# Performance work log

Hardware: AMD Instinct MI355X
Metric: run time of the kernel (lower is better)

## Reference

```python
import jax, jax.numpy as jnp
import numpy as np

B, T, D = 4, 2048, 1024
DEPTH = 4
LEAF_DIM = 256
NUM_LEAVES = 2 ** DEPTH          # 16
NUM_NODES = NUM_LEAVES - 1       # 15


def _uniform(key, shape, scale):
    s = 1.0 / np.sqrt(scale)
    return jax.random.uniform(key, shape, minval=-s, maxval=s, dtype=jnp.float32)


def setup_inputs() -> dict:
    key = jax.random.key(0)
    ks = jax.random.split(key, 8)
    x = jax.random.normal(ks[0], (B, T, D), dtype=jnp.float32)
    # gate params: Dense(1) per internal node, level-order layout
    node_w = _uniform(ks[1], (NUM_NODES, D), D)
    node_b = _uniform(ks[2], (NUM_NODES,), D)
    # leaf MLP params: D -> LEAF_DIM -> D, stacked over leaves
    w1 = _uniform(ks[3], (NUM_LEAVES, D, LEAF_DIM), D)
    b1 = _uniform(ks[4], (NUM_LEAVES, LEAF_DIM), D)
    w2 = _uniform(ks[5], (NUM_LEAVES, LEAF_DIM, D), LEAF_DIM)
    b2 = _uniform(ks[6], (NUM_LEAVES, D), LEAF_DIM)
    return {"x": x, "node_w": node_w, "node_b": node_b,
            "w1": w1, "b1": b1, "w2": w2, "b2": b2, "training": 0}


def _leaf_probs(x, node_w, node_b, depth):
    # gate activations for all internal nodes at once: [B,T,NUM_NODES]
    c = jax.nn.sigmoid(jnp.einsum('btd,nd->btn', x, node_w) + node_b)
    probs = jnp.ones(c.shape[:-1] + (1,), dtype=c.dtype)
    for m in range(depth):
        start = 2 ** m - 1
        cl = c[..., start:start + 2 ** m]          # gates at level m: [B,T,2^m]
        # left child gets c, right child gets (1-c); interleave preserves
        # the recursion's n -> (2n, 2n+1) indexing
        probs = jnp.stack([probs * cl, probs * (1.0 - cl)], axis=-1)
        probs = probs.reshape(probs.shape[:-2] + (-1,))
    return probs                                   # [B,T,NUM_LEAVES]


def reference(x, node_w, node_b, w1, b1, w2, b2, training):
    num_leaves = w1.shape[0]
    depth = int(np.log2(num_leaves))
    probs = _leaf_probs(x, node_w, node_b, depth)          # [B,T,L]
    # all leaf MLP hidden layers as one batched GEMM
    h = jax.nn.relu(jnp.einsum('btd,ldh->btlh', x, w1) + b1)
    # weight hidden by leaf probability, then contract l and h together so the
    # [B,T,L,D] per-leaf output is never materialized
    h = h * probs[..., None]
    out = jnp.einsum('btlh,lhd->btd', h, w2)
    out = out + jnp.einsum('btl,ld->btd', probs, b2)
    return out
```

## Files before the change

### kernel.cpp

```cpp
#include <hip/hip_runtime.h>
#include <stdint.h>

typedef unsigned short ushort_t;
typedef __bf16 bf16x8 __attribute__((ext_vector_type(8)));
typedef float f32x4 __attribute__((ext_vector_type(4)));

#define M_TOK 8192
#define K1 1024
#define N1 4096
#define K2 4160
#define N2 1024

template <int V> struct ic { static constexpr int value = V; };

__device__ __forceinline__ ushort_t f2bf(float f) {
  union { float f; unsigned u; } v; v.f = f;
  unsigned u = v.u;
  u += 0x7FFFu + ((u >> 16) & 1u);
  return (ushort_t)(u >> 16);
}

__device__ __forceinline__ void gload16(const void* g, void* l) {
  __builtin_amdgcn_global_load_lds((__attribute__((address_space(1))) void*)g,
                                   (__attribute__((address_space(3))) void*)l,
                                   16, 0, 0);
}

__global__ __launch_bounds__(256) void k_prep(
    const float* __restrict__ x, const float* __restrict__ node_w,
    const float* __restrict__ node_b, const float* __restrict__ w1,
    const float* __restrict__ w2, const float* __restrict__ b2,
    ushort_t* __restrict__ xb, float* __restrict__ probs,
    ushort_t* __restrict__ w1t, ushort_t* __restrict__ w2t,
    ushort_t* __restrict__ hp) {
  __shared__ ushort_t tile[64][68];
  const int b = blockIdx.x;
  if (b < 1024) {
    const int tr = threadIdx.x >> 4, tc = (threadIdx.x & 15) * 4;
    const int l = b >> 6, rem = b & 63;
    const int kt = rem >> 2, ht = rem & 3;
    const float* in = w1 + (size_t)l * K1 * 256;
#pragma unroll
    for (int rr = 0; rr < 4; ++rr) {
      int r = tr + rr * 16;
      float4 v = *(const float4*)(in + (size_t)(kt * 64 + r) * 256 + ht * 64 + tc);
      tile[r][tc+0] = f2bf(v.x); tile[r][tc+1] = f2bf(v.y);
      tile[r][tc+2] = f2bf(v.z); tile[r][tc+3] = f2bf(v.w);
    }
    __syncthreads();
#pragma unroll
    for (int rr = 0; rr < 4; ++rr) {
      int oh = tr + rr * 16;
      ushort4 o;
      o.x = tile[tc+0][oh]; o.y = tile[tc+1][oh];
      o.z = tile[tc+2][oh]; o.w = tile[tc+3][oh];
      *(ushort4*)(w1t + (size_t)(l * 256 + ht * 64 + oh) * K1 + kt * 64 + tc) = o;
    }
  } else if (b < 2048) {
    const int tr = threadIdx.x >> 4, tc = (threadIdx.x & 15) * 4;
    const int bb = b - 1024;
    const int l = bb >> 6, rem = bb & 63;
    const int ht = rem >> 4, dt = rem & 15;
    const float* in = w2 + (size_t)l * 256 * N2;
#pragma unroll
    for (int rr = 0; rr < 4; ++rr) {
      int r = tr + rr * 16;
      float4 v = *(const float4*)(in + (size_t)(ht * 64 + r) * N2 + dt * 64 + tc);
      tile[r][tc+0] = f2bf(v.x); tile[r][tc+1] = f2bf(v.y);
      tile[r][tc+2] = f2bf(v.z); tile[r][tc+3] = f2bf(v.w);
    }
    __syncthreads();
#pragma unroll
    for (int rr = 0; rr < 4; ++rr) {
      int od = tr + rr * 16;
      ushort4 o;
      o.x = tile[tc+0][od]; o.y = tile[tc+1][od];
      o.z = tile[tc+2][od]; o.w = tile[tc+3][od];
      *(ushort4*)(w2t + (size_t)(dt * 64 + od) * K2 + l * 256 + ht * 64 + tc) = o;
    }
  } else if (b < 2304) {
    int tid = (b - 2048) * 256 + threadIdx.x;
    int d = tid >> 6, cc = tid & 63;
    float v = (cc < 16) ? b2[cc * N2 + d] : 0.f;
    w2t[(size_t)d * K2 + 4096 + cc] = f2bf(v);
  } else {
    const int wid = threadIdx.x >> 6, lane = threadIdx.x & 63;
    const int t = (b - 2304) * 4 + wid;
    const float* xr = x + (size_t)t * K1;
    float xv[16];
#pragma unroll
    for (int j = 0; j < 4; ++j) {
      float4 v = *(const float4*)(xr + j * 256 + lane * 4);
      xv[4*j+0] = v.x; xv[4*j+1] = v.y; xv[4*j+2] = v.z; xv[4*j+3] = v.w;
    }
    ushort_t* xbr = xb + (size_t)t * K1;
#pragma unroll
    for (int j = 0; j < 4; ++j) {
      ushort4 o;
      o.x = f2bf(xv[4*j+0]); o.y = f2bf(xv[4*j+1]);
      o.z = f2bf(xv[4*j+2]); o.w = f2bf(xv[4*j+3]);
      *(ushort4*)(xbr + j * 256 + lane * 4) = o;
    }
    float c[15];
#pragma unroll
    for (int n = 0; n < 15; ++n) {
      float s = 0.f;
      const float* wr = node_w + n * K1;
#pragma unroll
      for (int j = 0; j < 4; ++j) {
        float4 w = *(const float4*)(wr + j * 256 + lane * 4);
        s += xv[4*j+0]*w.x + xv[4*j+1]*w.y + xv[4*j+2]*w.z + xv[4*j+3]*w.w;
      }
#pragma unroll
      for (int off = 32; off > 0; off >>= 1) s += __shfl_xor(s, off);
      float z = s + node_b[n];
      c[n] = 1.f / (1.f + __expf(-z));
    }
    if (lane < 16) {
      float p = 1.f;
#pragma unroll
      for (int m = 0; m < 4; ++m) {
        int jm = lane >> (4 - m);
        int node = (1 << m) - 1 + jm;
        int bit = (lane >> (3 - m)) & 1;
        p *= bit ? (1.f - c[node]) : c[node];
      }
      probs[t * 16 + lane] = p;
      hp[(size_t)t * K2 + 4096 + lane] = f2bf(p);
    }
    if (lane < 48) hp[(size_t)t * K2 + 4112 + lane] = 0;
  }
}

template <int NT, int LDA, int LDB, int BM, int BN, int THREADS, int MODE>
__global__ __launch_bounds__(THREADS, 4) void k_gemm(
    const ushort_t* __restrict__ A, const ushort_t* __restrict__ Bt,
    const float* __restrict__ probs, const float* __restrict__ b1,
    ushort_t* __restrict__ hp, float* __restrict__ out, int ntn) {
  constexpr int NWAVE = THREADS / 64;
  constexpr int WN = (BN == 256) ? 4 : 2;
  constexpr int WM = NWAVE / WN;
  constexpr int HA = BM / 2;
  constexpr int FH = HA / (WM * 16);
  constexpr int BHR = BN / 2;
  constexpr int ATILE = BM * 64;
  constexpr int BBYTES = BHR * 64;
  constexpr int BOFF = 2 * ATILE;
  constexpr int AR = (BM * 64) / (THREADS * 16);

  extern __shared__ char lds[];
  const int tid = threadIdx.x;
  int bid = blockIdx.x;
  const int nwg = gridDim.x;
  bid = (bid & 7) * (nwg >> 3) + (bid >> 3);
  const int bm = bid / ntn, bn = bid % ntn;

  const int wid = tid >> 6, lane = tid & 63;
  const int widM = wid / WN, widN = wid % WN;
  const int wmBase = widM * (FH * 16);
  const int wn = widN * 64;
  const int lr = lane & 15, g = lane >> 4;
  const int swz = (g ^ ((lr >> 1) & 3)) << 4;

  const ushort_t* Ag = A + (size_t)bm * BM * LDA;
  const ushort_t* Bg = Bt + (size_t)bn * BN * LDB;

  auto stageA = [&](int buf, int kt) {
#pragma unroll
    for (int r = 0; r < AR; ++r) {
      int srow = (tid >> 2) + r * (THREADS / 4);
      int scol = (((tid & 3) ^ ((srow >> 1) & 3)) << 4);
      gload16((const char*)(Ag + (size_t)srow * LDA) + kt * 64 + scol,
              lds + buf * ATILE + r * (THREADS * 16) + tid * 16);
    }
  };
  auto stageB = [&](int buf, int half, int kt) {
    int srow = tid >> 2;
    int scol = (((tid & 3) ^ ((srow >> 1) & 3)) << 4);
    gload16((const char*)(Bg + (size_t)(half * BHR + srow) * LDB) + kt * 64 + scol,
            lds + BOFF + (buf * 2 + half) * BBYTES + tid * 16);
  };
  auto rdA = [&](int buf, int half, int i) -> bf16x8 {
    int row = half * HA + wmBase + i * 16 + lr;
    return *(const bf16x8*)(lds + buf * ATILE + row * 64 + swz);
  };
  auto rdB = [&](int buf, int j) -> bf16x8 {
    int nr = wn + j * 16;
    int half = (nr >= BHR) ? 1 : 0;
    int r = (nr & (BHR - 1)) + lr;
    return *(const bf16x8*)(lds + BOFF + (buf * 2 + half) * BBYTES + r * 64 + swz);
  };

  f32x4 acc[2 * FH][4];
#pragma unroll
  for (int i = 0; i < 2 * FH; ++i)
#pragma unroll
    for (int j = 0; j < 4; ++j) acc[i][j] = (f32x4){0.f, 0.f, 0.f, 0.f};

  stageA(0, 0); stageB(0, 0, 0); stageB(0, 1, 0);
  stageB(1, 0, 1); stageB(1, 1, 1);
  asm volatile("s_waitcnt vmcnt(2)" ::: "memory");
  __builtin_amdgcn_sched_barrier(0);
  __builtin_amdgcn_s_barrier();
  __builtin_amdgcn_sched_barrier(0);

  auto body = [&](auto CURC, int kt) {
    constexpr int cur = decltype(CURC)::value;
    bf16x8 bfr[4];
    {
      bf16x8 a0[FH];
#pragma unroll
      for (int i = 0; i < FH; ++i) a0[i] = rdA(cur, 0, i);
#pragma unroll
      for (int j = 0; j < 4; ++j) bfr[j] = rdB(cur, j);
      if (kt + 1 < NT) stageA(cur ^ 1, kt + 1);
      __builtin_amdgcn_s_setprio(1);
#pragma unroll
      for (int j = 0; j < 4; ++j)
#pragma unroll
        for (int i = 0; i < FH; ++i)
          acc[i][j] = __builtin_amdgcn_mfma_f32_16x16x32_bf16(
              a0[i], bfr[j], acc[i][j], 0, 0, 0);
      __builtin_amdgcn_s_setprio(0);
    }
    __builtin_amdgcn_s_barrier();
    __builtin_amdgcn_sched_barrier(0);
    {
      bf16x8 a1[FH];
#pragma unroll
      for (int i = 0; i < FH; ++i) a1[i] = rdA(cur, 1, i);
      if (kt + 2 < NT) { stageB(cur, 0, kt + 2); stageB(cur, 1, kt + 2); }
      __builtin_amdgcn_s_setprio(1);
#pragma unroll
      for (int j = 0; j < 4; ++j)
#pragma unroll
        for (int i = 0; i < FH; ++i)
          acc[FH + i][j] = __builtin_amdgcn_mfma_f32_16x16x32_bf16(
              a1[i], bfr[j], acc[FH + i][j], 0, 0, 0);
      __builtin_amdgcn_s_setprio(0);
    }
    if (kt + 2 < NT) {
      asm volatile("s_waitcnt vmcnt(2)" ::: "memory");
      __builtin_amdgcn_sched_barrier(0);
    } else if (kt + 1 < NT) {
      asm volatile("s_waitcnt vmcnt(0)" ::: "memory");
      __builtin_amdgcn_sched_barrier(0);
    }
    __builtin_amdgcn_s_barrier();
    __builtin_amdgcn_sched_barrier(0);
  };

  int kt = 0;
#pragma unroll 1
  for (int it = 0; it < NT / 2; ++it) {
    body(ic<0>{}, kt); ++kt;
    body(ic<1>{}, kt); ++kt;
  }

  const int rowb = bm * BM + wmBase + g * 4;
  const int colb = bn * BN + wn + lr;
  if (MODE == 0) {
    const int leaf = bn;
#pragma unroll
    for (int q = 0; q < 2; ++q)
#pragma unroll
      for (int i = 0; i < FH; ++i) {
        int rbase = rowb + q * HA + i * 16;
        float pm[4];
#pragma unroll
        for (int rg = 0; rg < 4; ++rg)
          pm[rg] = probs[(size_t)(rbase + rg) * 16 + leaf];
#pragma unroll
        for (int j = 0; j < 4; ++j) {
          float bias = b1[colb + j * 16];
#pragma unroll
          for (int rg = 0; rg < 4; ++rg) {
            float v = acc[q * FH + i][j][rg] + bias;
            v = v > 0.f ? v : 0.f;
            v *= pm[rg];
            hp[(size_t)(rbase + rg) * K2 + colb + j * 16] = f2bf(v);
          }
        }
      }
  } else {
#pragma unroll
    for (int q = 0; q < 2; ++q)
#pragma unroll
      for (int i = 0; i < FH; ++i) {
        int rbase = rowb + q * HA + i * 16;
#pragma unroll
        for (int j = 0; j < 4; ++j)
#pragma unroll
          for (int rg = 0; rg < 4; ++rg)
            out[(size_t)(rbase + rg) * N2 + colb + j * 16] = acc[q * FH + i][j][rg];
      }
  }
}

extern "C" void kernel_launch(void* const* d_in, const int* in_sizes, int n_in,
                              void* d_out, int out_size, void* d_ws, size_t ws_size,
                              hipStream_t stream) {
  const float* x      = (const float*)d_in[0];
  const float* node_w = (const float*)d_in[1];
  const float* node_b = (const float*)d_in[2];
  const float* w1     = (const float*)d_in[3];
  const float* b1     = (const float*)d_in[4];
  const float* w2     = (const float*)d_in[5];
  const float* b2     = (const float*)d_in[6];
  float* out = (float*)d_out;

  char* ws = (char*)d_ws;
  ushort_t* xb    = (ushort_t*)(ws);
  ushort_t* w1t   = (ushort_t*)(ws + 16777216);
  ushort_t* w2t   = (ushort_t*)(ws + 25165824);
  ushort_t* hp    = (ushort_t*)(ws + 33685504);
  float*    probs = (float*)   (ws + 101842944);

  k_prep<<<4352, 256, 0, stream>>>(x, node_w, node_b, w1, w2, b2,
                                   xb, probs, w1t, w2t, hp);
  k_gemm<32, K1, K1, 128, 256, 512, 0><<<1024, 512, 49152, stream>>>(
      xb, w1t, probs, b1, hp, nullptr, N1 / 256);
  k_gemm<130, K2, K2, 128, 128, 256, 1><<<512, 256, 32768, stream>>>(
      hp, w2t, nullptr, nullptr, nullptr, out, N2 / 128);
}
```

Before: 188.5 us.

## Rewrite GEMMs with 256x128 tiles, K=64 steps and triple-buffered LDS pipeline

Replaces the templated GEMM with a fixed 256x128 tile, 512-thread kernel that loads 64-wide K slices into a three-stage LDS ring (144 KB) and prefetches register fragments for the next stage while doing MFMAs on the current one. Both GEMMs now use it: the first gets 1024 blocks of 256x128 and the second 256 blocks. The aim is to overlap global loads, LDS reads and MFMAs more deeply and to reuse each loaded tile more. In exchange, the large LDS footprint limits occupancy to about one block per CU, and the second GEMM's 256 blocks only roughly fill the device.

New measurement: 182.8 us. -3.0%, faster.

```diff
diff --git a/kernel.cpp b/kernel.cpp
--- a/kernel.cpp
+++ b/kernel.cpp
@@ -132,22 +132,14 @@
   }
 }
 
-template <int NT, int LDA, int LDB, int BM, int BN, int THREADS, int MODE>
-__global__ __launch_bounds__(THREADS, 4) void k_gemm(
+template <int NT, int LDA, int LDB, int MODE>
+__global__ __launch_bounds__(512, 2) void k_gemm3(
     const ushort_t* __restrict__ A, const ushort_t* __restrict__ Bt,
     const float* __restrict__ probs, const float* __restrict__ b1,
     ushort_t* __restrict__ hp, float* __restrict__ out, int ntn) {
-  constexpr int NWAVE = THREADS / 64;
-  constexpr int WN = (BN == 256) ? 4 : 2;
-  constexpr int WM = NWAVE / WN;
-  constexpr int HA = BM / 2;
-  constexpr int FH = HA / (WM * 16);
-  constexpr int BHR = BN / 2;
-  constexpr int ATILE = BM * 64;
-  constexpr int BBYTES = BHR * 64;
-  constexpr int BOFF = 2 * ATILE;
-  constexpr int AR = (BM * 64) / (THREADS * 16);
-
+  constexpr int ATILE = 256 * 128;
+  constexpr int BTILE = 128 * 128;
+  constexpr int TBYTES = ATILE + BTILE;
   extern __shared__ char lds[];
   const int tid = threadIdx.x;
   int bid = blockIdx.x;
@@ -156,144 +148,157 @@
   const int bm = bid / ntn, bn = bid % ntn;
 
   const int wid = tid >> 6, lane = tid & 63;
-  const int widM = wid / WN, widN = wid % WN;
-  const int wmBase = widM * (FH * 16);
-  const int wn = widN * 64;
+  const int widM = wid >> 1, widN = wid & 1;
   const int lr = lane & 15, g = lane >> 4;
-  const int swz = (g ^ ((lr >> 1) & 3)) << 4;
-
-  const ushort_t* Ag = A + (size_t)bm * BM * LDA;
-  const ushort_t* Bg = Bt + (size_t)bn * BN * LDB;
-
-  auto stageA = [&](int buf, int kt) {
-#pragma unroll
-    for (int r = 0; r < AR; ++r) {
-      int srow = (tid >> 2) + r * (THREADS / 4);
-      int scol = (((tid & 3) ^ ((srow >> 1) & 3)) << 4);
-      gload16((const char*)(Ag + (size_t)srow * LDA) + kt * 64 + scol,
-              lds + buf * ATILE + r * (THREADS * 16) + tid * 16);
+
+  const ushort_t* Ag = A + (size_t)bm * 256 * LDA;
+  const ushort_t* Bg = Bt + (size_t)bn * 128 * LDB;
+
+  auto stageHalf = [&](char* base, int kt, int part) {
+#pragma unroll
+    for (int r = 0; r < 2; ++r) {
+      int s = tid + part * 1024 + r * 512;
+      int row = s >> 3;
+      int c16 = (s & 7) ^ (row & 7);
+      gload16((const char*)(Ag + (size_t)row * LDA) + kt * 128 + (c16 << 4),
+              base + s * 16);
+    }
+    {
+      int s = tid + part * 512;
+      int row = s >> 3;
+      int c16 = (s & 7) ^ (row & 7);
+      gload16((const char*)(Bg + (size_t)row * LDB) + kt * 128 + (c16 << 4),
+              base + ATILE + s * 16);
     }
   };
-  auto stageB = [&](int buf, int half, int kt) {
-    int srow = tid >> 2;
-    int scol = (((tid & 3) ^ ((srow >> 1) & 3)) << 4);
-    gload16((const char*)(Bg + (size_t)(half * BHR + srow) * LDB) + kt * 64 + scol,
-            lds + BOFF + (buf * 2 + half) * BBYTES + tid * 16);
+  auto rdA = [&](char* base, int mi, int kk) -> bf16x8 {
+    int row = widM * 64 + mi * 16 + lr;
+    return *(const bf16x8*)(base + row * 128 + (((kk * 4 + g) ^ (lr & 7)) << 4));
   };
-  auto rdA = [&](int buf, int half, int i) -> bf16x8 {
-    int row = half * HA + wmBase + i * 16 + lr;
-    return *(const bf16x8*)(lds + buf * ATILE + row * 64 + swz);
+  auto rdB = [&](char* base, int nj, int kk) -> bf16x8 {
+    int row = widN * 64 + nj * 16 + lr;
+    return *(const bf16x8*)(base + ATILE + row * 128 + (((kk * 4 + g) ^ (lr & 7)) << 4));
   };
-  auto rdB = [&](int buf, int j) -> bf16x8 {
-    int nr = wn + j * 16;
-    int half = (nr >= BHR) ? 1 : 0;
-    int r = (nr & (BHR - 1)) + lr;
-    return *(const bf16x8*)(lds + BOFF + (buf * 2 + half) * BBYTES + r * 64 + swz);
-  };
-
-  f32x4 acc[2 * FH][4];
-#pragma unroll
-  for (int i = 0; i < 2 * FH; ++i)
+
+  f32x4 acc[4][4];
+#pragma unroll
+  for (int i = 0; i < 4; ++i)
 #pragma unroll
     for (int j = 0; j < 4; ++j) acc[i][j] = (f32x4){0.f, 0.f, 0.f, 0.f};
 
-  stageA(0, 0); stageB(0, 0, 0); stageB(0, 1, 0);
-  stageB(1, 0, 1); stageB(1, 1, 1);
-  asm volatile("s_waitcnt vmcnt(2)" ::: "memory");
+  bf16x8 a01[2][4];
+  bf16x8 bfr[2][8];
+  bf16x8 a23[4];
+
+  char* r0 = lds;
+  char* r1 = lds + TBYTES;
+  char* r2 = lds + 2 * TBYTES;
+
+  stageHalf(r0, 0, 0); stageHalf(r0, 0, 1);
+  stageHalf(r1, 1, 0); stageHalf(r1, 1, 1);
+  asm volatile("s_waitcnt vmcnt(6)" ::: "memory");
   __builtin_amdgcn_sched_barrier(0);
   __builtin_amdgcn_s_barrier();
   __builtin_amdgcn_sched_barrier(0);
-
-  auto body = [&](auto CURC, int kt) {
-    constexpr int cur = decltype(CURC)::value;
-    bf16x8 bfr[4];
-    {
-      bf16x8 a0[FH];
-#pragma unroll
-      for (int i = 0; i < FH; ++i) a0[i] = rdA(cur, 0, i);
-#pragma unroll
-      for (int j = 0; j < 4; ++j) bfr[j] = rdB(cur, j);
-      if (kt + 1 < NT) stageA(cur ^ 1, kt + 1);
-      __builtin_amdgcn_s_setprio(1);
-#pragma unroll
-      for (int j = 0; j < 4; ++j)
-#pragma unroll
-        for (int i = 0; i < FH; ++i)
-          acc[i][j] = __builtin_amdgcn_mfma_f32_16x16x32_bf16(
-              a0[i], bfr[j], acc[i][j], 0, 0, 0);
-      __builtin_amdgcn_s_setprio(0);
-    }
-    __builtin_amdgcn_s_barrier();
+#pragma unroll
+  for (int mi = 0; mi < 2; ++mi)
+#pragma unroll
+    for (int kk = 0; kk < 2; ++kk) a01[0][mi * 2 + kk] = rdA(r0, mi, kk);
+#pragma unroll
+  for (int nj = 0; nj < 4; ++nj)
+#pragma unroll
+    for (int kk = 0; kk < 2; ++kk) bfr[0][nj * 2 + kk] = rdB(r0, nj, kk);
+
+  auto body = [&](auto PARC, int kt, char* cur, char* nxt, char* stg) {
+    constexpr int P = decltype(PARC)::value;
+#pragma unroll
+    for (int mi = 0; mi < 2; ++mi)
+#pragma unroll
+      for (int kk = 0; kk < 2; ++kk) a23[mi * 2 + kk] = rdA(cur, mi + 2, kk);
+    if (kt + 2 < NT) stageHalf(stg, kt + 2, 0);
     __builtin_amdgcn_sched_barrier(0);
-    {
-      bf16x8 a1[FH];
-#pragma unroll
-      for (int i = 0; i < FH; ++i) a1[i] = rdA(cur, 1, i);
-      if (kt + 2 < NT) { stageB(cur, 0, kt + 2); stageB(cur, 1, kt + 2); }
-      __builtin_amdgcn_s_setprio(1);
-#pragma unroll
-      for (int j = 0; j < 4; ++j)
-#pragma unroll
-        for (int i = 0; i < FH; ++i)
-          acc[FH + i][j] = __builtin_amdgcn_mfma_f32_16x16x32_bf16(
-              a1[i], bfr[j], acc[FH + i][j], 0, 0, 0);
-      __builtin_amdgcn_s_setprio(0);
-    }
-    if (kt + 2 < NT) {
-      asm volatile("s_waitcnt vmcnt(2)" ::: "memory");
+    __builtin_amdgcn_s_setprio(1);
+#pragma unroll
+    for (int kk = 0; kk < 2; ++kk)
+#pragma unroll
+      for (int nj = 0; nj < 4; ++nj)
+#pragma unroll
+        for (int mi = 0; mi < 2; ++mi)
+          acc[mi][nj] = __builtin_amdgcn_mfma_f32_16x16x32_bf16(
+              a01[P][mi * 2 + kk], bfr[P][nj * 2 + kk], acc[mi][nj], 0, 0, 0);
+    __builtin_amdgcn_s_setprio(0);
+    if (kt + 1 < NT) {
+      if (kt + 2 < NT) asm volatile("s_waitcnt vmcnt(3)" ::: "memory");
+      else             asm volatile("s_waitcnt vmcnt(0)" ::: "memory");
       __builtin_amdgcn_sched_barrier(0);
-    } else if (kt + 1 < NT) {
-      asm volatile("s_waitcnt vmcnt(0)" ::: "memory");
+      __builtin_amdgcn_s_barrier();
       __builtin_amdgcn_sched_barrier(0);
-    }
-    __builtin_amdgcn_s_barrier();
+#pragma unroll
+      for (int mi = 0; mi < 2; ++mi)
+#pragma unroll
+        for (int kk = 0; kk < 2; ++kk) a01[P ^ 1][mi * 2 + kk] = rdA(nxt, mi, kk);
+#pragma unroll
+      for (int nj = 0; nj < 4; ++nj)
+#pragma unroll
+        for (int kk = 0; kk < 2; ++kk) bfr[P ^ 1][nj * 2 + kk] = rdB(nxt, nj, kk);
+      if (kt + 2 < NT) stageHalf(stg, kt + 2, 1);
+    }
     __builtin_amdgcn_sched_barrier(0);
+    __builtin_amdgcn_s_setprio(1);
+#pragma unroll
+    for (int kk = 0; kk < 2; ++kk)
+#pragma unroll
+      for (int nj = 0; nj < 4; ++nj)
+#pragma unroll
+        for (int mi = 0; mi < 2; ++mi)
+          acc[2 + mi][nj] = __builtin_amdgcn_mfma_f32_16x16x32_bf16(
+              a23[mi * 2 + kk], bfr[P][nj * 2 + kk], acc[2 + mi][nj], 0, 0, 0);
+    __builtin_amdgcn_s_setprio(0);
   };
 
   int kt = 0;
 #pragma unroll 1
   for (int it = 0; it < NT / 2; ++it) {
-    body(ic<0>{}, kt); ++kt;
-    body(ic<1>{}, kt); ++kt;
+    body(ic<0>{}, kt, r0, r1, r2); ++kt;
+    { char* t = r0; r0 = r1; r1 = r2; r2 = t; }
+    body(ic<1>{}, kt, r0, r1, r2); ++kt;
+    { char* t = r0; r0 = r1; r1 = r2; r2 = t; }
   }
-
-  const int rowb = bm * BM + wmBase + g * 4;
-  const int colb = bn * BN + wn + lr;
+  if constexpr (NT & 1) body(ic<0>{}, kt, r0, r1, r2);
+
+  const int rowb = bm * 256 + widM * 64 + g * 4;
+  const int colb = bn * 128 + widN * 64 + lr;
   if (MODE == 0) {
-    const int leaf = bn;
-#pragma unroll
-    for (int q = 0; q < 2; ++q)
-#pragma unroll
-      for (int i = 0; i < FH; ++i) {
-        int rbase = rowb + q * HA + i * 16;
-        float pm[4];
-#pragma unroll
-        for (int rg = 0; rg < 4; ++rg)
-          pm[rg] = probs[(size_t)(rbase + rg) * 16 + leaf];
-#pragma unroll
-        for (int j = 0; j < 4; ++j) {
-          float bias = b1[colb + j * 16];
-#pragma unroll
-          for (int rg = 0; rg < 4; ++rg) {
-            float v = acc[q * FH + i][j][rg] + bias;
-            v = v > 0.f ? v : 0.f;
-            v *= pm[rg];
-            hp[(size_t)(rbase + rg) * K2 + colb + j * 16] = f2bf(v);
-          }
+    const int leaf = bn >> 1;
+#pragma unroll
+    for (int mi = 0; mi < 4; ++mi) {
+      int rbase = rowb + mi * 16;
+      float pm[4];
+#pragma unroll
+      for (int rg = 0; rg < 4; ++rg)
+        pm[rg] = probs[(size_t)(rbase + rg) * 16 + leaf];
+#pragma unroll
+      for (int nj = 0; nj < 4; ++nj) {
+        float bias = b1[colb + nj * 16];
+#pragma unroll
+        for (int rg = 0; rg < 4; ++rg) {
+          float v = acc[mi][nj][rg] + bias;
+          v = v > 0.f ? v : 0.f;
+          v *= pm[rg];
+          hp[(size_t)(rbase + rg) * K2 + colb + nj * 16] = f2bf(v);
         }
       }
+    }
   } else {
 #pragma unroll
-    for (int q = 0; q < 2; ++q)
-#pragma unroll
-      for (int i = 0; i < FH; ++i) {
-        int rbase = rowb + q * HA + i * 16;
-#pragma unroll
-        for (int j = 0; j < 4; ++j)
-#pragma unroll
-          for (int rg = 0; rg < 4; ++rg)
-            out[(size_t)(rbase + rg) * N2 + colb + j * 16] = acc[q * FH + i][j][rg];
-      }
+    for (int mi = 0; mi < 4; ++mi) {
+      int rbase = rowb + mi * 16;
+#pragma unroll
+      for (int nj = 0; nj < 4; ++nj)
+#pragma unroll
+        for (int rg = 0; rg < 4; ++rg)
+          out[(size_t)(rbase + rg) * N2 + colb + nj * 16] = acc[mi][nj][rg];
+    }
   }
 }
 
@@ -318,8 +323,8 @@
 
   k_prep<<<4352, 256, 0, stream>>>(x, node_w, node_b, w1, w2, b2,
                                    xb, probs, w1t, w2t, hp);
-  k_gemm<32, K1, K1, 128, 256, 512, 0><<<1024, 512, 49152, stream>>>(
-      xb, w1t, probs, b1, hp, nullptr, N1 / 256);
-  k_gemm<130, K2, K2, 128, 128, 256, 1><<<512, 256, 32768, stream>>>(
+  k_gemm3<16, K1, K1, 0><<<1024, 512, 147456, stream>>>(
+      xb, w1t, probs, b1, hp, nullptr, N1 / 128);
+  k_gemm3<65, K2, K2, 1><<<256, 512, 147456, stream>>>(
       hp, w2t, nullptr, nullptr, nullptr, out, N2 / 128);
 }
```
